# Kernel optimization log

Hardware: AMD Instinct MI355X
Metric: run time of the kernel (lower is better)

The kernel has to match this reference:

```python
import jax, jax.numpy as jnp
import numpy as np

N_NODES = 50000
N_EDGES = 1600000
IN_F = 128
HEADS = 4
HEAD_DIM = 32  # out_features // heads = 128 // 4
NEG_SLOPE = 0.2


def setup_inputs() -> dict:
    key = jax.random.key(0)
    k1, k2, k3, k4 = jax.random.split(key, 4)
    x = jax.random.normal(k1, (N_NODES, IN_F), dtype=jnp.float32)
    edge_index = jax.random.randint(k2, (2, N_EDGES), 0, N_NODES, dtype=jnp.int64)
    # xavier-uniform-ish scaling for params
    W = jax.random.normal(k3, (HEADS * HEAD_DIM, IN_F), dtype=jnp.float32) * (1.0 / np.sqrt(IN_F))
    a = jax.random.normal(k4, (HEADS, 2 * HEAD_DIM), dtype=jnp.float32) * (1.0 / np.sqrt(2 * HEAD_DIM))
    return {"x": x, "edge_index": edge_index, "W": W, "a": a}


def reference(x, edge_index, W, a):
    # x: [N, F_in], edge_index: [2, E], W: [H*D, F_in], a: [H, 2D]
    N = x.shape[0]
    h = (x @ W.T).reshape(N, HEADS, HEAD_DIM)  # [N, H, D]
    src, dst = edge_index[0], edge_index[1]
    a_src = a[:, :HEAD_DIM]  # [H, D]
    a_dst = a[:, HEAD_DIM:]  # [H, D]
    h_src = h[src]  # [E, H, D]
    h_dst = h[dst]  # [E, H, D]
    # equivalent to (cat([h_src, h_dst], -1) * a).sum(-1), without materializing edge_h
    att = jnp.einsum('ehd,hd->eh', h_src, a_src) + jnp.einsum('ehd,hd->eh', h_dst, a_dst)
    att = jax.nn.leaky_relu(att, negative_slope=NEG_SLOPE)  # [E, H]
    msgs = att[..., None] * h_src  # [E, H, D]
    out = jax.ops.segment_sum(msgs, dst, num_segments=N)  # [N, H, D]
    # dropout is identity in eval/deterministic reference
    return out.reshape(N, HEADS * HEAD_DIM)
```

## Files before the change

kernel.cpp:

```cpp
#include <hip/hip_runtime.h>

#define N_NODES 50000
#define N_EDGES 1600000
#define IN_F 128
#define OUT_F 128
#define HEADS 4
#define HEAD_DIM 32
#define NEG_SLOPE 0.2f

#define NB 391
#define CAP 4800
#define P1_EPT 16
#define P1_EPB (P1_EPT * 256)

typedef __attribute__((ext_vector_type(8))) short short8v;
typedef __attribute__((ext_vector_type(4))) float f32x4;

__device__ __forceinline__ unsigned short f2bf(float f) {
    unsigned u = __builtin_bit_cast(unsigned, f);
    u += 0x7FFFu + ((u >> 16) & 1u);
    return (unsigned short)(u >> 16);
}
__device__ __forceinline__ float bf_lo(unsigned v) {
    return __builtin_bit_cast(float, v << 16);
}
__device__ __forceinline__ float bf_hi(unsigned v) {
    return __builtin_bit_cast(float, v & 0xFFFF0000u);
}

__global__ __launch_bounds__(256) void prep_kernel(
    const float* __restrict__ W, unsigned short* __restrict__ wbf,
    int* __restrict__ gcursor)
{
    int t = blockIdx.x * 256 + threadIdx.x;
    if (t < 16384) wbf[t] = f2bf(W[t]);
    if (t < NB) gcursor[t] = t * CAP;
}

__global__ __launch_bounds__(256) void gemm_mfma_kernel(
    const float* __restrict__ x, const unsigned short* __restrict__ wbf,
    const float* __restrict__ a,
    unsigned short* __restrict__ hb,
    float* __restrict__ alpha_s, float* __restrict__ alpha_d)
{
    const int tid = threadIdx.x;
    const int wave = tid >> 6;
    const int lane = tid & 63;
    const int lr = lane & 15;
    const int lg = lane >> 4;
    const int nodeA = blockIdx.x * 64 + wave * 16 + lr;
    const int nrow = nodeA < N_NODES ? nodeA : 0;

    f32x4 acc[8];
    #pragma unroll
    for (int i = 0; i < 8; ++i) acc[i] = (f32x4){0.f, 0.f, 0.f, 0.f};

    #pragma unroll
    for (int ks = 0; ks < 4; ++ks) {
        const float* xp = x + (size_t)nrow * 128 + ks * 32 + lg * 8;
        float4 xa = *(const float4*)xp;
        float4 xc = *(const float4*)(xp + 4);
        short8v afrag;
        afrag[0] = (short)f2bf(xa.x); afrag[1] = (short)f2bf(xa.y);
        afrag[2] = (short)f2bf(xa.z); afrag[3] = (short)f2bf(xa.w);
        afrag[4] = (short)f2bf(xc.x); afrag[5] = (short)f2bf(xc.y);
        afrag[6] = (short)f2bf(xc.z); afrag[7] = (short)f2bf(xc.w);
        #pragma unroll
        for (int nf = 0; nf < 8; ++nf) {
            const short8v bfrag = *(const short8v*)(wbf + (size_t)(nf * 16 + lr) * 128 + ks * 32 + lg * 8);
            acc[nf] = __builtin_amdgcn_mfma_f32_16x16x32_bf16(afrag, bfrag, acc[nf], 0, 0, 0);
        }
    }

    float as_c[8], ad_c[8];
    #pragma unroll
    for (int nf = 0; nf < 8; ++nf) {
        const int idx = (nf >> 1) * 64 + (nf & 1) * 16 + lr;
        as_c[nf] = a[idx];
        ad_c[nf] = a[idx + 32];
    }

    const int nbase = blockIdx.x * 64 + wave * 16 + lg * 4;
    #pragma unroll
    for (int reg = 0; reg < 4; ++reg) {
        const int n2 = nbase + reg;
        if (n2 < N_NODES) {
            unsigned short* hp = hb + (size_t)n2 * 128 + lr;
            #pragma unroll
            for (int nf = 0; nf < 8; ++nf)
                hp[nf * 16] = f2bf(acc[nf][reg]);
        }
        float sh[4], th[4];
        #pragma unroll
        for (int hd = 0; hd < 4; ++hd) {
            sh[hd] = acc[2 * hd][reg] * as_c[2 * hd] + acc[2 * hd + 1][reg] * as_c[2 * hd + 1];
            th[hd] = acc[2 * hd][reg] * ad_c[2 * hd] + acc[2 * hd + 1][reg] * ad_c[2 * hd + 1];
        }
        #pragma unroll
        for (int off = 8; off >= 1; off >>= 1) {
            #pragma unroll
            for (int hd = 0; hd < 4; ++hd) {
                sh[hd] += __shfl_xor(sh[hd], off);
                th[hd] += __shfl_xor(th[hd], off);
            }
        }
        if (lr == 0 && n2 < N_NODES) {
            #pragma unroll
            for (int hd = 0; hd < 4; ++hd) {
                alpha_s[n2 * 4 + hd] = sh[hd];
                alpha_d[n2 * 4 + hd] = th[hd];
            }
        }
    }
}

__global__ __launch_bounds__(256) void part_kernel(
    const int* __restrict__ ei, int* __restrict__ gcursor,
    unsigned* __restrict__ part)
{
    __shared__ int cnt[NB];
    __shared__ int gbase[NB];
    const int tid = threadIdx.x;
    const int e0 = blockIdx.x * P1_EPB;

    for (int i = tid; i < NB; i += 256) cnt[i] = 0;
    __syncthreads();

    unsigned pk[P1_EPT];
    int bk[P1_EPT];
    int loc[P1_EPT];
    #pragma unroll
    for (int c4 = 0; c4 < P1_EPT / 4; ++c4) {
        int e = e0 + c4 * 1024 + tid * 4;
        if (e < N_EDGES) {
            int4 s4 = *(const int4*)(ei + e);
            int4 d4 = *(const int4*)(ei + N_EDGES + e);
            int ss[4] = {s4.x, s4.y, s4.z, s4.w};
            int dd[4] = {d4.x, d4.y, d4.z, d4.w};
            #pragma unroll
            for (int j = 0; j < 4; ++j) {
                int k = c4 * 4 + j;
                int bb = dd[j] >> 7;
                bk[k] = bb;
                pk[k] = ((unsigned)(dd[j] & 127) << 16) | (unsigned)ss[j];
                loc[k] = atomicAdd(&cnt[bb], 1);
            }
        } else {
            #pragma unroll
            for (int j = 0; j < 4; ++j) bk[c4 * 4 + j] = -1;
        }
    }
    __syncthreads();
    for (int bq = tid; bq < NB; bq += 256)
        gbase[bq] = atomicAdd(&gcursor[bq], cnt[bq]);
    __syncthreads();
    #pragma unroll
    for (int k = 0; k < P1_EPT; ++k)
        if (bk[k] >= 0)
            part[gbase[bk[k]] + loc[k]] = pk[k];
}

__global__ __launch_bounds__(256) void bucket_kernel(
    const int* __restrict__ gcursor, const unsigned* __restrict__ part,
    unsigned short* __restrict__ srcs16,
    int* __restrict__ node_start, int* __restrict__ node_cnt)
{
    __shared__ unsigned ent[CAP];
    __shared__ unsigned short srt[CAP];
    __shared__ int cnt4[4][128];
    __shared__ int sc[128];
    __shared__ int cur4[4][128];

    const int b = blockIdx.x;
    const int tid = threadIdx.x;
    const int w = tid >> 6;
    const int bstart = b * CAP;
    int n_b = gcursor[b] - bstart;
    if (n_b > CAP) n_b = CAP;

    if (tid < 128) {
        cnt4[0][tid] = 0; cnt4[1][tid] = 0; cnt4[2][tid] = 0; cnt4[3][tid] = 0;
    }
    __syncthreads();

    for (int i = tid; i < n_b; i += 256) {
        unsigned e = part[bstart + i];
        ent[i] = e;
        atomicAdd(&cnt4[w][e >> 16], 1);
    }
    __syncthreads();

    int c = 0;
    if (tid < 128) {
        c = cnt4[0][tid] + cnt4[1][tid] + cnt4[2][tid] + cnt4[3][tid];
        sc[tid] = c;
    }
    __syncthreads();
    #pragma unroll
    for (int off = 1; off < 128; off <<= 1) {
        int v = 0;
        if (tid < 128 && tid >= off) v = sc[tid - off];
        __syncthreads();
        if (tid < 128) sc[tid] += v;
        __syncthreads();
    }
    if (tid < 128) {
        int eb = sc[tid] - c;
        int c0 = cnt4[0][tid], c1 = cnt4[1][tid], c2 = cnt4[2][tid];
        cur4[0][tid] = eb;
        cur4[1][tid] = eb + c0;
        cur4[2][tid] = eb + c0 + c1;
        cur4[3][tid] = eb + c0 + c1 + c2;
        const int node = b * 128 + tid;
        if (node < N_NODES) {
            node_start[node] = bstart + eb;
            node_cnt[node] = c;
        }
    }
    __syncthreads();

    for (int i = tid; i < n_b; i += 256) {
        unsigned e = ent[i];
        int loc = atomicAdd(&cur4[w][e >> 16], 1);
        srt[loc] = (unsigned short)(e & 0xFFFFu);
    }
    __syncthreads();

    const unsigned* srt32 = (const unsigned*)srt;
    unsigned* dst32 = (unsigned*)(srcs16 + bstart);
    const int nw2 = (n_b + 1) >> 1;
    for (int i = tid; i < nw2; i += 256) dst32[i] = srt32[i];
}

__global__ __launch_bounds__(256) void gather_kernel(
    const unsigned short* __restrict__ srcs,
    const int* __restrict__ node_start, const int* __restrict__ node_cnt,
    const unsigned* __restrict__ h32,
    const float* __restrict__ alpha_s, const float* __restrict__ alpha_d,
    float* __restrict__ out)
{
    const int wid = (blockIdx.x * 256 + threadIdx.x) >> 6;
    if (wid >= N_NODES) return;
    const int lane = threadIdx.x & 63;
    const int start = node_start[wid];
    const int end = start + node_cnt[wid];
    const int head = lane >> 4;

    const float adv = alpha_d[wid * 4 + head];

    float a0x = 0.f, a0y = 0.f, a1x = 0.f, a1y = 0.f;
    float a2x = 0.f, a2y = 0.f, a3x = 0.f, a3y = 0.f;
    int i = start;
    for (; i + 7 < end; i += 8) {
        int s0 = srcs[i],     s1 = srcs[i + 1], s2 = srcs[i + 2], s3 = srcs[i + 3];
        int s4 = srcs[i + 4], s5 = srcs[i + 5], s6 = srcs[i + 6], s7 = srcs[i + 7];
        float t0 = alpha_s[s0 * 4 + head] + adv;
        float t1 = alpha_s[s1 * 4 + head] + adv;
        float t2 = alpha_s[s2 * 4 + head] + adv;
        float t3 = alpha_s[s3 * 4 + head] + adv;
        float t4 = alpha_s[s4 * 4 + head] + adv;
        float t5 = alpha_s[s5 * 4 + head] + adv;
        float t6 = alpha_s[s6 * 4 + head] + adv;
        float t7 = alpha_s[s7 * 4 + head] + adv;
        t0 = t0 > 0.f ? t0 : NEG_SLOPE * t0;
        t1 = t1 > 0.f ? t1 : NEG_SLOPE * t1;
        t2 = t2 > 0.f ? t2 : NEG_SLOPE * t2;
        t3 = t3 > 0.f ? t3 : NEG_SLOPE * t3;
        t4 = t4 > 0.f ? t4 : NEG_SLOPE * t4;
        t5 = t5 > 0.f ? t5 : NEG_SLOPE * t5;
        t6 = t6 > 0.f ? t6 : NEG_SLOPE * t6;
        t7 = t7 > 0.f ? t7 : NEG_SLOPE * t7;
        unsigned v0 = h32[(size_t)s0 * 64 + lane];
        unsigned v1 = h32[(size_t)s1 * 64 + lane];
        unsigned v2 = h32[(size_t)s2 * 64 + lane];
        unsigned v3 = h32[(size_t)s3 * 64 + lane];
        unsigned v4 = h32[(size_t)s4 * 64 + lane];
        unsigned v5 = h32[(size_t)s5 * 64 + lane];
        unsigned v6 = h32[(size_t)s6 * 64 + lane];
        unsigned v7 = h32[(size_t)s7 * 64 + lane];
        a0x = fmaf(t0, bf_lo(v0), a0x); a0y = fmaf(t0, bf_hi(v0), a0y);
        a1x = fmaf(t1, bf_lo(v1), a1x); a1y = fmaf(t1, bf_hi(v1), a1y);
        a2x = fmaf(t2, bf_lo(v2), a2x); a2y = fmaf(t2, bf_hi(v2), a2y);
        a3x = fmaf(t3, bf_lo(v3), a3x); a3y = fmaf(t3, bf_hi(v3), a3y);
        a0x = fmaf(t4, bf_lo(v4), a0x); a0y = fmaf(t4, bf_hi(v4), a0y);
        a1x = fmaf(t5, bf_lo(v5), a1x); a1y = fmaf(t5, bf_hi(v5), a1y);
        a2x = fmaf(t6, bf_lo(v6), a2x); a2y = fmaf(t6, bf_hi(v6), a2y);
        a3x = fmaf(t7, bf_lo(v7), a3x); a3y = fmaf(t7, bf_hi(v7), a3y);
    }
    for (; i + 1 < end; i += 2) {
        int s0 = srcs[i], s1 = srcs[i + 1];
        float t0 = alpha_s[s0 * 4 + head] + adv;
        float t1 = alpha_s[s1 * 4 + head] + adv;
        t0 = t0 > 0.f ? t0 : NEG_SLOPE * t0;
        t1 = t1 > 0.f ? t1 : NEG_SLOPE * t1;
        unsigned v0 = h32[(size_t)s0 * 64 + lane];
        unsigned v1 = h32[(size_t)s1 * 64 + lane];
        a0x = fmaf(t0, bf_lo(v0), a0x); a0y = fmaf(t0, bf_hi(v0), a0y);
        a1x = fmaf(t1, bf_lo(v1), a1x); a1y = fmaf(t1, bf_hi(v1), a1y);
    }
    if (i < end) {
        int s0 = srcs[i];
        float t0 = alpha_s[s0 * 4 + head] + adv;
        t0 = t0 > 0.f ? t0 : NEG_SLOPE * t0;
        unsigned v0 = h32[(size_t)s0 * 64 + lane];
        a2x = fmaf(t0, bf_lo(v0), a2x); a2y = fmaf(t0, bf_hi(v0), a2y);
    }
    float2 r = {(a0x + a1x) + (a2x + a3x), (a0y + a1y) + (a2y + a3y)};
    ((float2*)out)[(size_t)wid * 64 + lane] = r;
}

__global__ __launch_bounds__(256) void edge_kernel(
    const int* __restrict__ ei,
    const unsigned* __restrict__ h32,
    const float* __restrict__ alpha_s, const float* __restrict__ alpha_d,
    float* __restrict__ out)
{
    const unsigned total = (unsigned)N_EDGES * 32u;
    const unsigned stride = gridDim.x * blockDim.x;
    for (unsigned i = blockIdx.x * blockDim.x + threadIdx.x; i < total; i += stride) {
        const int e = (int)(i >> 5);
        const int c = (int)(i & 31);
        const int src = ei[e];
        const int dst = ei[N_EDGES + e];
        const int head = c >> 3;

        float att = alpha_s[src * 4 + head] + alpha_d[dst * 4 + head];
        att = att > 0.f ? att : NEG_SLOPE * att;

        unsigned v0 = h32[(size_t)src * 64 + c * 2];
        unsigned v1 = h32[(size_t)src * 64 + c * 2 + 1];
        float* po = out + (size_t)dst * 128 + c * 4;
        atomicAdd(po + 0, att * bf_lo(v0));
        atomicAdd(po + 1, att * bf_hi(v0));
        atomicAdd(po + 2, att * bf_lo(v1));
        atomicAdd(po + 3, att * bf_hi(v1));
    }
}

extern "C" void kernel_launch(void* const* d_in, const int* in_sizes, int n_in,
                              void* d_out, int out_size, void* d_ws, size_t ws_size,
                              hipStream_t stream) {
    const float* x  = (const float*)d_in[0];
    const int*   ei = (const int*)d_in[1];
    const float* W  = (const float*)d_in[2];
    const float* a  = (const float*)d_in[3];
    float* out = (float*)d_out;

    unsigned short* hb = (unsigned short*)d_ws;
    float* as = (float*)(hb + (size_t)N_NODES * 128);
    float* ad = as + (size_t)N_NODES * 4;
    unsigned* part = (unsigned*)(ad + (size_t)N_NODES * 4);
    unsigned short* srcs16 = (unsigned short*)(part + (size_t)NB * CAP);
    int* gcursor = (int*)(srcs16 + (size_t)NB * CAP);
    int* node_start = gcursor + 512;
    int* node_cnt   = node_start + 50176;
    unsigned short* wbf = (unsigned short*)(node_cnt + 50176);
    const size_t needed = (size_t)((char*)(wbf + 16384) - (char*)d_ws);

    prep_kernel<<<64, 256, 0, stream>>>(W, wbf, gcursor);
    gemm_mfma_kernel<<<(N_NODES + 63) / 64, 256, 0, stream>>>(x, wbf, a, hb, as, ad);

    if (ws_size >= needed) {
        part_kernel<<<(N_EDGES + P1_EPB - 1) / P1_EPB, 256, 0, stream>>>(ei, gcursor, part);
        bucket_kernel<<<NB, 256, 0, stream>>>(gcursor, part, srcs16, node_start, node_cnt);
        gather_kernel<<<(N_NODES * 64 + 255) / 256, 256, 0, stream>>>(
            srcs16, node_start, node_cnt, (const unsigned*)hb, as, ad, out);
    } else {
        hipMemsetAsync(d_out, 0, (size_t)out_size * sizeof(float), stream);
        edge_kernel<<<4096, 256, 0, stream>>>(ei, (const unsigned*)hb, as, ad, out);
    }
}
```

Baseline: 121.4 us.

## Precompute per-edge attention in bucket kernel and stream it in gather

Moves the leaky-ReLU attention computation from the gather kernel into the bucket kernel, which writes bf16-packed per-edge attention for all four heads in sorted order (att01 reuses the part buffer after it has been read into shared memory, att23 is a new buffer). The gather kernel then reads attention contiguously instead of doing random alpha_s lookups per edge, and uses 32-bit index arithmetic. CAP is reduced slightly, presumably to fit shared memory or the workspace. The trade-off is extra writes in bucket, random as4 reads moved there, and bf16 rounding of the attention values.

```diff
diff --git a/kernel.cpp b/kernel.cpp
--- a/kernel.cpp
+++ b/kernel.cpp
@@ -9,7 +9,7 @@
 #define NEG_SLOPE 0.2f
 
 #define NB 391
-#define CAP 4800
+#define CAP 4792
 #define P1_EPT 16
 #define P1_EPB (P1_EPT * 256)
 
@@ -26,6 +26,9 @@
 }
 __device__ __forceinline__ float bf_hi(unsigned v) {
     return __builtin_bit_cast(float, v & 0xFFFF0000u);
+}
+__device__ __forceinline__ float bfu(unsigned short u) {
+    return __builtin_bit_cast(float, (unsigned)u << 16);
 }
 
 __global__ __launch_bounds__(256) void prep_kernel(
@@ -163,6 +166,8 @@
 __global__ __launch_bounds__(256) void bucket_kernel(
     const int* __restrict__ gcursor, const unsigned* __restrict__ part,
     unsigned short* __restrict__ srcs16,
+    unsigned* __restrict__ att01, unsigned* __restrict__ att23,
+    const float4* __restrict__ as4, const float4* __restrict__ ad4,
     int* __restrict__ node_start, int* __restrict__ node_cnt)
 {
     __shared__ unsigned ent[CAP];
@@ -221,8 +226,19 @@
 
     for (int i = tid; i < n_b; i += 256) {
         unsigned e = ent[i];
-        int loc = atomicAdd(&cur4[w][e >> 16], 1);
-        srt[loc] = (unsigned short)(e & 0xFFFFu);
+        int ln = (int)(e >> 16);
+        int loc = atomicAdd(&cur4[w][ln], 1);
+        unsigned srcid = e & 0xFFFFu;
+        srt[loc] = (unsigned short)srcid;
+        float4 sv = as4[srcid];
+        float4 dv = ad4[b * 128 + ln];
+        float t0 = sv.x + dv.x, t1 = sv.y + dv.y, t2 = sv.z + dv.z, t3 = sv.w + dv.w;
+        t0 = t0 > 0.f ? t0 : NEG_SLOPE * t0;
+        t1 = t1 > 0.f ? t1 : NEG_SLOPE * t1;
+        t2 = t2 > 0.f ? t2 : NEG_SLOPE * t2;
+        t3 = t3 > 0.f ? t3 : NEG_SLOPE * t3;
+        att01[bstart + loc] = (unsigned)f2bf(t0) | ((unsigned)f2bf(t1) << 16);
+        att23[bstart + loc] = (unsigned)f2bf(t2) | ((unsigned)f2bf(t3) << 16);
     }
     __syncthreads();
 
@@ -236,48 +252,40 @@
     const unsigned short* __restrict__ srcs,
     const int* __restrict__ node_start, const int* __restrict__ node_cnt,
     const unsigned* __restrict__ h32,
-    const float* __restrict__ alpha_s, const float* __restrict__ alpha_d,
+    const unsigned* __restrict__ att01, const unsigned* __restrict__ att23,
     float* __restrict__ out)
 {
     const int wid = (blockIdx.x * 256 + threadIdx.x) >> 6;
     if (wid >= N_NODES) return;
-    const int lane = threadIdx.x & 63;
-    const int start = node_start[wid];
-    const int end = start + node_cnt[wid];
-    const int head = lane >> 4;
-
-    const float adv = alpha_d[wid * 4 + head];
+    const unsigned lane = threadIdx.x & 63;
+    const unsigned start = (unsigned)node_start[wid];
+    const unsigned end = start + (unsigned)node_cnt[wid];
+    const unsigned hsel = (lane >> 4) & 1;
+    const unsigned short* __restrict__ ab =
+        (const unsigned short*)((lane & 32) ? att23 : att01);
 
     float a0x = 0.f, a0y = 0.f, a1x = 0.f, a1y = 0.f;
     float a2x = 0.f, a2y = 0.f, a3x = 0.f, a3y = 0.f;
-    int i = start;
-    for (; i + 7 < end; i += 8) {
-        int s0 = srcs[i],     s1 = srcs[i + 1], s2 = srcs[i + 2], s3 = srcs[i + 3];
-        int s4 = srcs[i + 4], s5 = srcs[i + 5], s6 = srcs[i + 6], s7 = srcs[i + 7];
-        float t0 = alpha_s[s0 * 4 + head] + adv;
-        float t1 = alpha_s[s1 * 4 + head] + adv;
-        float t2 = alpha_s[s2 * 4 + head] + adv;
-        float t3 = alpha_s[s3 * 4 + head] + adv;
-        float t4 = alpha_s[s4 * 4 + head] + adv;
-        float t5 = alpha_s[s5 * 4 + head] + adv;
-        float t6 = alpha_s[s6 * 4 + head] + adv;
-        float t7 = alpha_s[s7 * 4 + head] + adv;
-        t0 = t0 > 0.f ? t0 : NEG_SLOPE * t0;
-        t1 = t1 > 0.f ? t1 : NEG_SLOPE * t1;
-        t2 = t2 > 0.f ? t2 : NEG_SLOPE * t2;
-        t3 = t3 > 0.f ? t3 : NEG_SLOPE * t3;
-        t4 = t4 > 0.f ? t4 : NEG_SLOPE * t4;
-        t5 = t5 > 0.f ? t5 : NEG_SLOPE * t5;
-        t6 = t6 > 0.f ? t6 : NEG_SLOPE * t6;
-        t7 = t7 > 0.f ? t7 : NEG_SLOPE * t7;
-        unsigned v0 = h32[(size_t)s0 * 64 + lane];
-        unsigned v1 = h32[(size_t)s1 * 64 + lane];
-        unsigned v2 = h32[(size_t)s2 * 64 + lane];
-        unsigned v3 = h32[(size_t)s3 * 64 + lane];
-        unsigned v4 = h32[(size_t)s4 * 64 + lane];
-        unsigned v5 = h32[(size_t)s5 * 64 + lane];
-        unsigned v6 = h32[(size_t)s6 * 64 + lane];
-        unsigned v7 = h32[(size_t)s7 * 64 + lane];
+    unsigned i = start;
+    for (; i + 8 <= end; i += 8) {
+        unsigned s0 = srcs[i],     s1 = srcs[i + 1], s2 = srcs[i + 2], s3 = srcs[i + 3];
+        unsigned s4 = srcs[i + 4], s5 = srcs[i + 5], s6 = srcs[i + 6], s7 = srcs[i + 7];
+        float t0 = bfu(ab[((i + 0) << 1) | hsel]);
+        float t1 = bfu(ab[((i + 1) << 1) | hsel]);
+        float t2 = bfu(ab[((i + 2) << 1) | hsel]);
+        float t3 = bfu(ab[((i + 3) << 1) | hsel]);
+        float t4 = bfu(ab[((i + 4) << 1) | hsel]);
+        float t5 = bfu(ab[((i + 5) << 1) | hsel]);
+        float t6 = bfu(ab[((i + 6) << 1) | hsel]);
+        float t7 = bfu(ab[((i + 7) << 1) | hsel]);
+        unsigned v0 = h32[(s0 << 6) | lane];
+        unsigned v1 = h32[(s1 << 6) | lane];
+        unsigned v2 = h32[(s2 << 6) | lane];
+        unsigned v3 = h32[(s3 << 6) | lane];
+        unsigned v4 = h32[(s4 << 6) | lane];
+        unsigned v5 = h32[(s5 << 6) | lane];
+        unsigned v6 = h32[(s6 << 6) | lane];
+        unsigned v7 = h32[(s7 << 6) | lane];
         a0x = fmaf(t0, bf_lo(v0), a0x); a0y = fmaf(t0, bf_hi(v0), a0y);
         a1x = fmaf(t1, bf_lo(v1), a1x); a1y = fmaf(t1, bf_hi(v1), a1y);
         a2x = fmaf(t2, bf_lo(v2), a2x); a2y = fmaf(t2, bf_hi(v2), a2y);
@@ -287,26 +295,23 @@
         a2x = fmaf(t6, bf_lo(v6), a2x); a2y = fmaf(t6, bf_hi(v6), a2y);
         a3x = fmaf(t7, bf_lo(v7), a3x); a3y = fmaf(t7, bf_hi(v7), a3y);
     }
-    for (; i + 1 < end; i += 2) {
-        int s0 = srcs[i], s1 = srcs[i + 1];
-        float t0 = alpha_s[s0 * 4 + head] + adv;
-        float t1 = alpha_s[s1 * 4 + head] + adv;
-        t0 = t0 > 0.f ? t0 : NEG_SLOPE * t0;
-        t1 = t1 > 0.f ? t1 : NEG_SLOPE * t1;
-        unsigned v0 = h32[(size_t)s0 * 64 + lane];
-        unsigned v1 = h32[(size_t)s1 * 64 + lane];
+    for (; i + 2 <= end; i += 2) {
+        unsigned s0 = srcs[i], s1 = srcs[i + 1];
+        float t0 = bfu(ab[((i + 0) << 1) | hsel]);
+        float t1 = bfu(ab[((i + 1) << 1) | hsel]);
+        unsigned v0 = h32[(s0 << 6) | lane];
+        unsigned v1 = h32[(s1 << 6) | lane];
         a0x = fmaf(t0, bf_lo(v0), a0x); a0y = fmaf(t0, bf_hi(v0), a0y);
         a1x = fmaf(t1, bf_lo(v1), a1x); a1y = fmaf(t1, bf_hi(v1), a1y);
     }
     if (i < end) {
-        int s0 = srcs[i];
-        float t0 = alpha_s[s0 * 4 + head] + adv;
-        t0 = t0 > 0.f ? t0 : NEG_SLOPE * t0;
-        unsigned v0 = h32[(size_t)s0 * 64 + lane];
+        unsigned s0 = srcs[i];
+        float t0 = bfu(ab[(i << 1) | hsel]);
+        unsigned v0 = h32[(s0 << 6) | lane];
         a2x = fmaf(t0, bf_lo(v0), a2x); a2y = fmaf(t0, bf_hi(v0), a2y);
     }
     float2 r = {(a0x + a1x) + (a2x + a3x), (a0y + a1y) + (a2y + a3y)};
-    ((float2*)out)[(size_t)wid * 64 + lane] = r;
+    ((float2*)out)[(unsigned)wid * 64 + lane] = r;
 }
 
 __global__ __launch_bounds__(256) void edge_kernel(
@@ -351,7 +356,8 @@
     float* ad = as + (size_t)N_NODES * 4;
     unsigned* part = (unsigned*)(ad + (size_t)N_NODES * 4);
     unsigned short* srcs16 = (unsigned short*)(part + (size_t)NB * CAP);
-    int* gcursor = (int*)(srcs16 + (size_t)NB * CAP);
+    unsigned* att23 = (unsigned*)(srcs16 + (size_t)NB * CAP);
+    int* gcursor = (int*)(att23 + (size_t)NB * CAP);
     int* node_start = gcursor + 512;
     int* node_cnt   = node_start + 50176;
     unsigned short* wbf = (unsigned short*)(node_cnt + 50176);
@@ -362,9 +368,12 @@
 
     if (ws_size >= needed) {
         part_kernel<<<(N_EDGES + P1_EPB - 1) / P1_EPB, 256, 0, stream>>>(ei, gcursor, part);
-        bucket_kernel<<<NB, 256, 0, stream>>>(gcursor, part, srcs16, node_start, node_cnt);
+        bucket_kernel<<<NB, 256, 0, stream>>>(
+            gcursor, part, srcs16, part, att23,
+            (const float4*)as, (const float4*)ad, node_start, node_cnt);
         gather_kernel<<<(N_NODES * 64 + 255) / 256, 256, 0, stream>>>(
-            srcs16, node_start, node_cnt, (const unsigned*)hb, as, ad, out);
+            srcs16, node_start, node_cnt, (const unsigned*)hb,
+            part, att23, out);
     } else {
         hipMemsetAsync(d_out, 0, (size_t)out_size * sizeof(float), stream);
         edge_kernel<<<4096, 256, 0, stream>>>(ei, (const unsigned*)hb, as, ad, out);
```

Result: slower. 137.0 us (+12.9%).
